# Optimization experiments

Measured on AMD Instinct MI355X. Metric: run time of the kernel, lower is better.

The kernel has to match this reference:

```python
import jax, jax.numpy as jnp
import numpy as np

ALPHA = 2.0   # ATan surrogate sharpness (spikingjelly default)
V_TH = 1.0    # spike threshold

@jax.custom_vjp
def spike(v):
    # Heaviside spike at threshold V_TH
    return (v >= V_TH).astype(v.dtype)

def _spike_fwd(v):
    return spike(v), v

def _spike_bwd(v, g):
    # ATan surrogate gradient
    sg = (ALPHA / 2.0) / (1.0 + (jnp.pi / 2.0 * ALPHA * (v - V_TH)) ** 2)
    return (g * sg,)

spike.defvjp(_spike_fwd, _spike_bwd)

N, T, D_IN, HID, D_OUT = 512, 1000, 128, 128, 20

def _linear_params(k, fan_in, fan_out):
    # matches torch nn.Linear default init: U(-1/sqrt(fan_in), 1/sqrt(fan_in))
    s = 1.0 / np.sqrt(fan_in)
    kw, kb = jax.random.split(k)
    W = jax.random.uniform(kw, (fan_out, fan_in), minval=-s, maxval=s, dtype=jnp.float32)
    b = jax.random.uniform(kb, (fan_out,), minval=-s, maxval=s, dtype=jnp.float32)
    return W, b

def setup_inputs() -> dict:
    key = jax.random.key(0)
    kx, k1, k2, k3, k4, k5 = jax.random.split(key, 6)
    x = jax.random.normal(kx, (N, T, D_IN), dtype=jnp.float32)
    Wi1, bi1 = _linear_params(k1, D_IN, HID)   # i2h_1
    Wh1, bh1 = _linear_params(k2, HID, HID)    # h2h_1
    Wi2, bi2 = _linear_params(k3, HID, HID)    # i2h_2
    Wh2, bh2 = _linear_params(k4, HID, HID)    # h2h_2
    Wo,  bo  = _linear_params(k5, HID, D_OUT)  # h2o_2
    return {"x": x, "Wi1": Wi1, "bi1": bi1, "Wh1": Wh1, "bh1": bh1,
            "Wi2": Wi2, "bi2": bi2, "Wh2": Wh2, "bh2": bh2, "Wo": Wo, "bo": bo}

def reference(x, Wi1, bi1, Wh1, bh1, Wi2, bi2, Wh2, bh2, Wo, bo):
    n, t = x.shape[0], x.shape[1]
    s1_0 = jnp.zeros((n, Wh1.shape[0]), dtype=x.dtype)
    s2_0 = jnp.zeros((n, Wh2.shape[0]), dtype=x.dtype)
    acc0 = jnp.zeros((n, Wo.shape[0]), dtype=x.dtype)

    def step(carry, xt):
        s1, s2, acc = carry
        h1 = xt @ Wi1.T + bi1 + s1 @ Wh1.T + bh1
        s1 = spike(h1)
        h2 = s1 @ Wi2.T + bi2 + s2 @ Wh2.T + bh2
        s2 = spike(h2)
        acc = acc + s2 @ Wo.T + bo
        return (s1, s2, acc), None

    # scan over time: x -> [T, N, D_IN]
    (_, _, acc), _ = jax.lax.scan(step, (s1_0, s2_0, acc0), jnp.swapaxes(x, 0, 1))
    return acc / t
```

## Files before the change

### kernel.cpp

```cpp
#include <hip/hip_runtime.h>
#include <cstdint>
#include <cstddef>

#define T_STEPS 1000
#define NS      512
#define HID     128
#define DOUT    20
#define XPAD    129
#define PSTR    130
#define SPMM_R  32

extern "C" __global__ void __launch_bounds__(512, 1)
srnn_dense(const float* __restrict__ x, const float* __restrict__ Wi1,
           float* __restrict__ D, int t0, int Tc)
{
    extern __shared__ float sm[];
    float* xs = sm;
    float* Wl = sm + 128 * XPAD;
    const int tid = threadIdx.x;
    const int w = tid >> 6, ln = tid & 63;
    const int rb = blockIdx.x * 128;

    for (int i = tid; i < HID * HID / 4; i += 512)
        ((float4*)Wl)[i] = ((const float4*)Wi1)[i];
    for (int i = tid; i < 128 * 32; i += 512) {
        int r = i >> 5, kq = i & 31;
        int cr = rb + r;
        int s = cr / Tc, trel = cr - s * Tc;
        float4 v = ((const float4*)x)[((size_t)s * T_STEPS + t0 + trel) * 32 + kq];
        float* dst = &xs[r * XPAD + 4 * kq];
        dst[0] = v.x; dst[1] = v.y; dst[2] = v.z; dst[3] = v.w;
    }
    __syncthreads();

    const float* xr0 = xs + ln * XPAD;
    const float* xr1 = xs + (64 + ln) * XPAD;
    for (int og = 0; og < 4; ++og) {
        const int o = 16 * w + 4 * og;
        float a[2][4][4];
        #pragma unroll
        for (int r = 0; r < 2; ++r)
            #pragma unroll
            for (int j = 0; j < 4; ++j)
                #pragma unroll
                for (int i = 0; i < 4; ++i) a[r][j][i] = 0.f;

        #pragma unroll 4
        for (int k = 0; k < HID; k += 4) {
            float4 wv[4];
            #pragma unroll
            for (int j = 0; j < 4; ++j)
                wv[j] = *(const float4*)&Wl[(o + j) * HID + k];
            float xa0[4], xa1[4];
            #pragma unroll
            for (int i = 0; i < 4; ++i) { xa0[i] = xr0[k + i]; xa1[i] = xr1[k + i]; }
            #pragma unroll
            for (int j = 0; j < 4; ++j) {
                a[0][j][0] = fmaf(xa0[0], wv[j].x, a[0][j][0]);
                a[0][j][1] = fmaf(xa0[1], wv[j].y, a[0][j][1]);
                a[0][j][2] = fmaf(xa0[2], wv[j].z, a[0][j][2]);
                a[0][j][3] = fmaf(xa0[3], wv[j].w, a[0][j][3]);
                a[1][j][0] = fmaf(xa1[0], wv[j].x, a[1][j][0]);
                a[1][j][1] = fmaf(xa1[1], wv[j].y, a[1][j][1]);
                a[1][j][2] = fmaf(xa1[2], wv[j].z, a[1][j][2]);
                a[1][j][3] = fmaf(xa1[3], wv[j].w, a[1][j][3]);
            }
        }
        #pragma unroll
        for (int r = 0; r < 2; ++r) {
            float4 dv;
            dv.x = (a[r][0][0] + a[r][0][1]) + (a[r][0][2] + a[r][0][3]);
            dv.y = (a[r][1][0] + a[r][1][1]) + (a[r][1][2] + a[r][1][3]);
            dv.z = (a[r][2][0] + a[r][2][1]) + (a[r][2][2] + a[r][2][3]);
            dv.w = (a[r][3][0] + a[r][3][1]) + (a[r][3][2] + a[r][3][3]);
            *(float4*)&D[(size_t)(rb + 64 * r + ln) * HID + o] = dv;
        }
    }
}

__device__ __forceinline__ void stage_paired(float* __restrict__ WT2,
                                             const float* __restrict__ W,
                                             int tid, int nthreads)
{
    for (int i = tid; i < HID * HID / 4; i += nthreads) {
        int o = i >> 5, jq = i & 31;
        float4 v = ((const float4*)W)[i];
        int c = 2 * (o & 63) + (o >> 6);
        WT2[(4 * jq + 0) * PSTR + c] = v.x;
        WT2[(4 * jq + 1) * PSTR + c] = v.y;
        WT2[(4 * jq + 2) * PSTR + c] = v.z;
        WT2[(4 * jq + 3) * PSTR + c] = v.w;
    }
    for (int i = tid; i < PSTR; i += nthreads) WT2[128 * PSTR + i] = 0.f;
}

__device__ __forceinline__ void sparse4p(const float* __restrict__ WT2,
                                         unsigned long long mm, int base,
                                         int ln2, float& rl, float& rh)
{
    while (mm) {
        int j0 = (int)__builtin_ctzll(mm) + base;            mm &= mm - 1;
        int j1 = mm ? (int)__builtin_ctzll(mm) + base : 128; mm &= mm - 1;
        int j2 = mm ? (int)__builtin_ctzll(mm) + base : 128; mm &= mm - 1;
        int j3 = mm ? (int)__builtin_ctzll(mm) + base : 128; mm &= mm - 1;
        float2 p0 = *(const float2*)&WT2[j0 * PSTR + ln2];
        float2 p1 = *(const float2*)&WT2[j1 * PSTR + ln2];
        float2 p2 = *(const float2*)&WT2[j2 * PSTR + ln2];
        float2 p3 = *(const float2*)&WT2[j3 * PSTR + ln2];
        rl += p0.x; rl += p1.x; rl += p2.x; rl += p3.x;
        rh += p0.y; rh += p1.y; rh += p2.y; rh += p3.y;
    }
}

extern "C" __global__ void __launch_bounds__(128, 1)
srnn_recur1(const float* __restrict__ Dn, const float* __restrict__ Wh,
            const float* __restrict__ bi, const float* __restrict__ bh,
            ulonglong2* __restrict__ masks, ulonglong2* __restrict__ state,
            int t0, int Tc, int first)
{
    extern __shared__ float WT2[];
    const int tid = threadIdx.x, w = tid >> 6, ln = tid & 63, ln2 = 2 * ln;
    const int s = 2 * blockIdx.x + w;

    stage_paired(WT2, Wh, tid, 128);

    const float bil = bi[ln], bih = bi[64 + ln];
    const float bhl = bh[ln], bhh = bh[64 + ln];
    unsigned long long m0 = 0ULL, m1 = 0ULL;
    if (!first) { ulonglong2 st = state[s]; m0 = st.x; m1 = st.y; }

    const float* Drow = Dn + (size_t)s * Tc * HID;
    float dl[8], dh[8];
    #pragma unroll
    for (int p = 0; p < 8; ++p) {
        int ti = p < Tc ? p : Tc - 1;
        dl[p] = Drow[ti * HID + ln];
        dh[p] = Drow[ti * HID + 64 + ln];
    }
    __syncthreads();

    for (int tt = 0; tt < Tc; tt += 8) {
        #pragma unroll
        for (int u = 0; u < 8; ++u) {
            int t = tt + u;
            if (t >= Tc) break;
            float dense_l = dl[u], dense_h = dh[u];
            int tp = (t + 8 < Tc) ? t + 8 : Tc - 1;
            dl[u] = Drow[tp * HID + ln];
            dh[u] = Drow[tp * HID + 64 + ln];

            float rl = 0.f, rh = 0.f;
            sparse4p(WT2, m0, 0,  ln2, rl, rh);
            sparse4p(WT2, m1, 64, ln2, rl, rh);

            float hl = ((dense_l + bil) + rl) + bhl;
            float hh = ((dense_h + bih) + rh) + bhh;
            m0 = __ballot(hl >= 1.0f);
            m1 = __ballot(hh >= 1.0f);
            if (ln == 0) {
                ulonglong2 mv; mv.x = m0; mv.y = m1;
                masks[(size_t)s * T_STEPS + (t0 + t)] = mv;
            }
        }
    }
    if (ln == 0) { ulonglong2 st; st.x = m0; st.y = m1; state[s] = st; }
}

extern "C" __global__ void __launch_bounds__(256, 1)
srnn_spmm(const ulonglong2* __restrict__ masks1, const float* __restrict__ Wi2,
          float* __restrict__ D2, int t0, int Tc)
{
    extern __shared__ float WI2[];
    const int tid = threadIdx.x, w = tid >> 6, ln = tid & 63, ln2 = 2 * ln;
    stage_paired(WI2, Wi2, tid, 256);
    __syncthreads();

    const int s = blockIdx.y;
    const int tbase = (blockIdx.x * 4 + w) * SPMM_R;
    if (tbase >= Tc) return;
    const ulonglong2* mrow = masks1 + (size_t)s * T_STEPS + t0;

    ulonglong2 m = mrow[tbase];
    for (int r = 0; r < SPMM_R; ++r) {
        int trel = tbase + r;
        if (trel >= Tc) break;
        ulonglong2 cm = m;
        if (r + 1 < SPMM_R && trel + 1 < Tc) m = mrow[trel + 1];

        float Al = 0.f, Ah = 0.f;
        sparse4p(WI2, cm.x, 0,  ln2, Al, Ah);
        sparse4p(WI2, cm.y, 64, ln2, Al, Ah);

        size_t ro = ((size_t)s * Tc + trel) * HID;
        D2[ro + ln] = Al;
        D2[ro + 64 + ln] = Ah;
    }
}

extern "C" __global__ void __launch_bounds__(128, 1)
srnn_recur2(const float* __restrict__ D2, const float* __restrict__ Wh2,
            const float* __restrict__ bi2, const float* __restrict__ bh2,
            const float* __restrict__ Wo,  const float* __restrict__ bo,
            ulonglong2* __restrict__ state, float* __restrict__ accst,
            float* __restrict__ out, int t0, int Tc, int first, int last)
{
    extern __shared__ float sm2[];
    float* WT2 = sm2;
    float* WOt = sm2 + 129 * PSTR;
    const int tid = threadIdx.x, w = tid >> 6, ln = tid & 63, ln2 = 2 * ln;
    const int s = 2 * blockIdx.x + w;

    stage_paired(WT2, Wh2, tid, 128);
    for (int i = tid; i < DOUT * HID / 4; i += 128) {
        int o = i >> 5, jq = i & 31;
        float4 v = ((const float4*)Wo)[i];
        WOt[(4 * jq + 0) * DOUT + o] = v.x; WOt[(4 * jq + 1) * DOUT + o] = v.y;
        WOt[(4 * jq + 2) * DOUT + o] = v.z; WOt[(4 * jq + 3) * DOUT + o] = v.w;
    }
    for (int i = tid; i < DOUT; i += 128) WOt[128 * DOUT + i] = 0.f;

    const float bil = bi2[ln], bih = bi2[64 + ln];
    const float bhl = bh2[ln], bhh = bh2[64 + ln];
    const bool  oth = (ln < DOUT);
    const float bov = oth ? bo[ln] : 0.f;
    unsigned long long p0 = 0ULL, p1 = 0ULL;
    float acc = 0.f;
    if (!first) {
        ulonglong2 st = state[s]; p0 = st.x; p1 = st.y;
        if (oth) acc = accst[s * DOUT + ln];
    }

    const float* Drow = D2 + (size_t)s * Tc * HID;
    float dl[8], dh[8];
    #pragma unroll
    for (int p = 0; p < 8; ++p) {
        int ti = p < Tc ? p : Tc - 1;
        dl[p] = Drow[ti * HID + ln];
        dh[p] = Drow[ti * HID + 64 + ln];
    }
    __syncthreads();

    for (int tt = 0; tt < Tc; tt += 8) {
        #pragma unroll
        for (int u = 0; u < 8; ++u) {
            int t = tt + u;
            if (t >= Tc) break;
            float Al = dl[u], Ah = dh[u];
            int tp = (t + 8 < Tc) ? t + 8 : Tc - 1;
            dl[u] = Drow[tp * HID + ln];
            dh[u] = Drow[tp * HID + 64 + ln];

            float Bl = 0.f, Bh = 0.f;
            sparse4p(WT2, p0, 0,  ln2, Bl, Bh);
            sparse4p(WT2, p1, 64, ln2, Bl, Bh);

            float hl = ((Al + bil) + Bl) + bhl;
            float hh = ((Ah + bih) + Bh) + bhh;
            p0 = __ballot(hl >= 1.0f);
            p1 = __ballot(hh >= 1.0f);

            if (oth) {
                float d = 0.f;
                unsigned long long mm = p0;
                while (mm) {
                    int j0 = (int)__builtin_ctzll(mm);       mm &= mm - 1;
                    int j1 = mm ? (int)__builtin_ctzll(mm) : 128; mm &= mm - 1;
                    int j2 = mm ? (int)__builtin_ctzll(mm) : 128; mm &= mm - 1;
                    int j3 = mm ? (int)__builtin_ctzll(mm) : 128; mm &= mm - 1;
                    float w0 = WOt[j0 * DOUT + ln], w1 = WOt[j1 * DOUT + ln];
                    float w2 = WOt[j2 * DOUT + ln], w3 = WOt[j3 * DOUT + ln];
                    d += w0; d += w1; d += w2; d += w3;
                }
                mm = p1;
                while (mm) {
                    int j0 = 64 + (int)__builtin_ctzll(mm);       mm &= mm - 1;
                    int j1 = mm ? 64 + (int)__builtin_ctzll(mm) : 128; mm &= mm - 1;
                    int j2 = mm ? 64 + (int)__builtin_ctzll(mm) : 128; mm &= mm - 1;
                    int j3 = mm ? 64 + (int)__builtin_ctzll(mm) : 128; mm &= mm - 1;
                    float w0 = WOt[j0 * DOUT + ln], w1 = WOt[j1 * DOUT + ln];
                    float w2 = WOt[j2 * DOUT + ln], w3 = WOt[j3 * DOUT + ln];
                    d += w0; d += w1; d += w2; d += w3;
                }
                acc += d;
                acc += bov;
            }
        }
    }
    if (ln == 0) { ulonglong2 st; st.x = p0; st.y = p1; state[s] = st; }
    if (oth) {
        if (last) out[s * DOUT + ln] = acc / (float)T_STEPS;
        else      accst[s * DOUT + ln] = acc;
    }
}

extern "C" void kernel_launch(void* const* d_in, const int* in_sizes, int n_in,
                              void* d_out, int out_size, void* d_ws, size_t ws_size,
                              hipStream_t stream) {
    const float* x   = (const float*)d_in[0];
    const float* Wi1 = (const float*)d_in[1];
    const float* bi1 = (const float*)d_in[2];
    const float* Wh1 = (const float*)d_in[3];
    const float* bh1 = (const float*)d_in[4];
    const float* Wi2 = (const float*)d_in[5];
    const float* bi2 = (const float*)d_in[6];
    const float* Wh2 = (const float*)d_in[7];
    const float* bh2 = (const float*)d_in[8];
    const float* Wo  = (const float*)d_in[9];
    const float* bo  = (const float*)d_in[10];
    float* out = (float*)d_out;

    const size_t mb = (size_t)NS * T_STEPS * sizeof(ulonglong2);
    ulonglong2* masks1 = (ulonglong2*)d_ws;
    ulonglong2* state  = (ulonglong2*)((char*)d_ws + mb);
    const size_t state_bytes = (size_t)2 * NS * sizeof(ulonglong2);
    float* accst = (float*)((char*)d_ws + mb + state_bytes);
    const size_t acc_bytes = (size_t)NS * DOUT * sizeof(float);
    float* Dbuf = (float*)((char*)d_ws + mb + state_bytes + acc_bytes);

    const size_t base = mb + state_bytes + acc_bytes;
    size_t avail = ws_size > base ? ws_size - base : 0;
    const size_t bytes_per_t = (size_t)NS * HID * sizeof(float);
    long tcmax = (long)(avail / bytes_per_t);
    static const int divs[] = {1000, 500, 250, 200, 125, 100, 50, 40, 25, 20, 10, 8, 5, 4, 2, 1};
    int Tc = 1;
    for (int i = 0; i < 16; ++i) if (divs[i] <= tcmax) { Tc = divs[i]; break; }

    const int lds0 = (128 * XPAD + HID * HID) * (int)sizeof(float);
    const int ldsP = (129 * PSTR) * (int)sizeof(float);
    const int lds2 = (129 * PSTR + 129 * DOUT) * (int)sizeof(float);
    hipFuncSetAttribute((const void*)srnn_dense,
                        hipFuncAttributeMaxDynamicSharedMemorySize, lds0);
    hipFuncSetAttribute((const void*)srnn_recur1,
                        hipFuncAttributeMaxDynamicSharedMemorySize, ldsP);
    hipFuncSetAttribute((const void*)srnn_spmm,
                        hipFuncAttributeMaxDynamicSharedMemorySize, ldsP);
    hipFuncSetAttribute((const void*)srnn_recur2,
                        hipFuncAttributeMaxDynamicSharedMemorySize, lds2);

    for (int t0 = 0; t0 < T_STEPS; t0 += Tc) {
        srnn_dense<<<4 * Tc, 512, lds0, stream>>>(x, Wi1, Dbuf, t0, Tc);
        srnn_recur1<<<NS / 2, 128, ldsP, stream>>>(Dbuf, Wh1, bi1, bh1,
                                                   masks1, state, t0, Tc, t0 == 0);
    }
    for (int t0 = 0; t0 < T_STEPS; t0 += Tc) {
        dim3 g2((Tc + 4 * SPMM_R - 1) / (4 * SPMM_R), NS);
        srnn_spmm<<<g2, 256, ldsP, stream>>>(masks1, Wi2, Dbuf, t0, Tc);
        srnn_recur2<<<NS / 2, 128, lds2, stream>>>(Dbuf, Wh2, bi2, bh2, Wo, bo,
                                                   state + NS, accst, out,
                                                   t0, Tc, t0 == 0,
                                                   t0 + Tc >= T_STEPS);
    }
}
```

Measured before the change: 1.800 ms.

## Software-pipeline sparse recurrent gathers by issuing next-step weight loads right after ballot

The two recurrent kernels now walk the spike bits of both mask halves through one merged iterator. Right after each ballot they gather the first eight weight rows for the next step, so those LDS loads overlap the mask store, the output accumulation and the next dense-input prefetch. The output projection in layer two reuses the same indices and hoists its first eight loads. The dense prefetch depth drops from 8 to 4 in a rolling register window, and Tc is limited to multiples of 4 to match the unroll. The register pressure is higher, and inactive lanes now run the output loop with a clamped column index.

```diff
diff --git a/kernel.cpp b/kernel.cpp
--- a/kernel.cpp
+++ b/kernel.cpp
@@ -94,6 +94,13 @@
     for (int i = tid; i < PSTR; i += nthreads) WT2[128 * PSTR + i] = 0.f;
 }
 
+__device__ __forceinline__ int popnext(unsigned long long& a, unsigned long long& b)
+{
+    if (a) { int j = (int)__builtin_ctzll(a); a &= a - 1; return j; }
+    if (b) { int j = 64 + (int)__builtin_ctzll(b); b &= b - 1; return j; }
+    return 128;
+}
+
 __device__ __forceinline__ void sparse4p(const float* __restrict__ WT2,
                                          unsigned long long mm, int base,
                                          int ln2, float& rl, float& rh)
@@ -128,40 +135,73 @@
     const float bhl = bh[ln], bhh = bh[64 + ln];
     unsigned long long m0 = 0ULL, m1 = 0ULL;
     if (!first) { ulonglong2 st = state[s]; m0 = st.x; m1 = st.y; }
+    __syncthreads();
 
     const float* Drow = Dn + (size_t)s * Tc * HID;
-    float dl[8], dh[8];
-    #pragma unroll
-    for (int p = 0; p < 8; ++p) {
-        int ti = p < Tc ? p : Tc - 1;
-        dl[p] = Drow[ti * HID + ln];
-        dh[p] = Drow[ti * HID + 64 + ln];
-    }
-    __syncthreads();
-
-    for (int tt = 0; tt < Tc; tt += 8) {
-        #pragma unroll
-        for (int u = 0; u < 8; ++u) {
-            int t = tt + u;
-            if (t >= Tc) break;
-            float dense_l = dl[u], dense_h = dh[u];
-            int tp = (t + 8 < Tc) ? t + 8 : Tc - 1;
-            dl[u] = Drow[tp * HID + ln];
-            dh[u] = Drow[tp * HID + 64 + ln];
-
-            float rl = 0.f, rh = 0.f;
-            sparse4p(WT2, m0, 0,  ln2, rl, rh);
-            sparse4p(WT2, m1, 64, ln2, rl, rh);
-
-            float hl = ((dense_l + bil) + rl) + bhl;
-            float hh = ((dense_h + bih) + rh) + bhh;
-            m0 = __ballot(hl >= 1.0f);
-            m1 = __ballot(hh >= 1.0f);
-            if (ln == 0) {
-                ulonglong2 mv; mv.x = m0; mv.y = m1;
-                masks[(size_t)s * T_STEPS + (t0 + t)] = mv;
-            }
-        }
+    const int i1 = 1 < Tc ? 1 : Tc - 1;
+    const int i2 = 2 < Tc ? 2 : Tc - 1;
+    const int i3 = 3 < Tc ? 3 : Tc - 1;
+    float cl0 = Drow[ln],            ch0 = Drow[64 + ln];
+    float cl1 = Drow[i1 * HID + ln], ch1 = Drow[i1 * HID + 64 + ln];
+    float cl2 = Drow[i2 * HID + ln], ch2 = Drow[i2 * HID + 64 + ln];
+    float cl3 = Drow[i3 * HID + ln], ch3 = Drow[i3 * HID + 64 + ln];
+
+    unsigned long long a = m0, b = m1;
+    int j0 = popnext(a, b), j1 = popnext(a, b), j2 = popnext(a, b), j3 = popnext(a, b);
+    int j4 = popnext(a, b), j5 = popnext(a, b), j6 = popnext(a, b), j7 = popnext(a, b);
+    float2 v0 = *(const float2*)&WT2[j0 * PSTR + ln2];
+    float2 v1 = *(const float2*)&WT2[j1 * PSTR + ln2];
+    float2 v2 = *(const float2*)&WT2[j2 * PSTR + ln2];
+    float2 v3 = *(const float2*)&WT2[j3 * PSTR + ln2];
+    float2 v4 = *(const float2*)&WT2[j4 * PSTR + ln2];
+    float2 v5 = *(const float2*)&WT2[j5 * PSTR + ln2];
+    float2 v6 = *(const float2*)&WT2[j6 * PSTR + ln2];
+    float2 v7 = *(const float2*)&WT2[j7 * PSTR + ln2];
+    unsigned long long ra = a, rb = b;
+
+    #pragma unroll 4
+    for (int t = 0; t < Tc; ++t) {
+        float rl = 0.f, rh = 0.f;
+        rl += v0.x; rl += v1.x; rl += v2.x; rl += v3.x;
+        rl += v4.x; rl += v5.x; rl += v6.x; rl += v7.x;
+        rh += v0.y; rh += v1.y; rh += v2.y; rh += v3.y;
+        rh += v4.y; rh += v5.y; rh += v6.y; rh += v7.y;
+        while (ra | rb) {
+            int k0 = popnext(ra, rb), k1 = popnext(ra, rb);
+            int k2 = popnext(ra, rb), k3 = popnext(ra, rb);
+            float2 q0 = *(const float2*)&WT2[k0 * PSTR + ln2];
+            float2 q1 = *(const float2*)&WT2[k1 * PSTR + ln2];
+            float2 q2 = *(const float2*)&WT2[k2 * PSTR + ln2];
+            float2 q3 = *(const float2*)&WT2[k3 * PSTR + ln2];
+            rl += q0.x; rl += q1.x; rl += q2.x; rl += q3.x;
+            rh += q0.y; rh += q1.y; rh += q2.y; rh += q3.y;
+        }
+
+        float hl = ((cl0 + bil) + rl) + bhl;
+        float hh = ((ch0 + bih) + rh) + bhh;
+        m0 = __ballot(hl >= 1.0f);
+        m1 = __ballot(hh >= 1.0f);
+        if (ln == 0) {
+            ulonglong2 mv; mv.x = m0; mv.y = m1;
+            masks[(size_t)s * T_STEPS + (t0 + t)] = mv;
+        }
+
+        a = m0; b = m1;
+        j0 = popnext(a, b); j1 = popnext(a, b); j2 = popnext(a, b); j3 = popnext(a, b);
+        j4 = popnext(a, b); j5 = popnext(a, b); j6 = popnext(a, b); j7 = popnext(a, b);
+        v0 = *(const float2*)&WT2[j0 * PSTR + ln2];
+        v1 = *(const float2*)&WT2[j1 * PSTR + ln2];
+        v2 = *(const float2*)&WT2[j2 * PSTR + ln2];
+        v3 = *(const float2*)&WT2[j3 * PSTR + ln2];
+        v4 = *(const float2*)&WT2[j4 * PSTR + ln2];
+        v5 = *(const float2*)&WT2[j5 * PSTR + ln2];
+        v6 = *(const float2*)&WT2[j6 * PSTR + ln2];
+        v7 = *(const float2*)&WT2[j7 * PSTR + ln2];
+        ra = a; rb = b;
+
+        cl0 = cl1; ch0 = ch1; cl1 = cl2; ch1 = ch2; cl2 = cl3; ch2 = ch3;
+        int tn = (t + 4 < Tc) ? t + 4 : Tc - 1;
+        cl3 = Drow[tn * HID + ln]; ch3 = Drow[tn * HID + 64 + ln];
     }
     if (ln == 0) { ulonglong2 st; st.x = m0; st.y = m1; state[s] = st; }
 }
@@ -222,6 +262,7 @@
     const float bil = bi2[ln], bih = bi2[64 + ln];
     const float bhl = bh2[ln], bhh = bh2[64 + ln];
     const bool  oth = (ln < DOUT);
+    const int   c   = oth ? ln : 0;
     const float bov = oth ? bo[ln] : 0.f;
     unsigned long long p0 = 0ULL, p1 = 0ULL;
     float acc = 0.f;
@@ -229,62 +270,85 @@
         ulonglong2 st = state[s]; p0 = st.x; p1 = st.y;
         if (oth) acc = accst[s * DOUT + ln];
     }
+    __syncthreads();
 
     const float* Drow = D2 + (size_t)s * Tc * HID;
-    float dl[8], dh[8];
-    #pragma unroll
-    for (int p = 0; p < 8; ++p) {
-        int ti = p < Tc ? p : Tc - 1;
-        dl[p] = Drow[ti * HID + ln];
-        dh[p] = Drow[ti * HID + 64 + ln];
-    }
-    __syncthreads();
-
-    for (int tt = 0; tt < Tc; tt += 8) {
-        #pragma unroll
-        for (int u = 0; u < 8; ++u) {
-            int t = tt + u;
-            if (t >= Tc) break;
-            float Al = dl[u], Ah = dh[u];
-            int tp = (t + 8 < Tc) ? t + 8 : Tc - 1;
-            dl[u] = Drow[tp * HID + ln];
-            dh[u] = Drow[tp * HID + 64 + ln];
-
-            float Bl = 0.f, Bh = 0.f;
-            sparse4p(WT2, p0, 0,  ln2, Bl, Bh);
-            sparse4p(WT2, p1, 64, ln2, Bl, Bh);
-
-            float hl = ((Al + bil) + Bl) + bhl;
-            float hh = ((Ah + bih) + Bh) + bhh;
-            p0 = __ballot(hl >= 1.0f);
-            p1 = __ballot(hh >= 1.0f);
-
-            if (oth) {
-                float d = 0.f;
-                unsigned long long mm = p0;
-                while (mm) {
-                    int j0 = (int)__builtin_ctzll(mm);       mm &= mm - 1;
-                    int j1 = mm ? (int)__builtin_ctzll(mm) : 128; mm &= mm - 1;
-                    int j2 = mm ? (int)__builtin_ctzll(mm) : 128; mm &= mm - 1;
-                    int j3 = mm ? (int)__builtin_ctzll(mm) : 128; mm &= mm - 1;
-                    float w0 = WOt[j0 * DOUT + ln], w1 = WOt[j1 * DOUT + ln];
-                    float w2 = WOt[j2 * DOUT + ln], w3 = WOt[j3 * DOUT + ln];
-                    d += w0; d += w1; d += w2; d += w3;
-                }
-                mm = p1;
-                while (mm) {
-                    int j0 = 64 + (int)__builtin_ctzll(mm);       mm &= mm - 1;
-                    int j1 = mm ? 64 + (int)__builtin_ctzll(mm) : 128; mm &= mm - 1;
-                    int j2 = mm ? 64 + (int)__builtin_ctzll(mm) : 128; mm &= mm - 1;
-                    int j3 = mm ? 64 + (int)__builtin_ctzll(mm) : 128; mm &= mm - 1;
-                    float w0 = WOt[j0 * DOUT + ln], w1 = WOt[j1 * DOUT + ln];
-                    float w2 = WOt[j2 * DOUT + ln], w3 = WOt[j3 * DOUT + ln];
-                    d += w0; d += w1; d += w2; d += w3;
-                }
-                acc += d;
-                acc += bov;
-            }
-        }
+    const int i1 = 1 < Tc ? 1 : Tc - 1;
+    const int i2 = 2 < Tc ? 2 : Tc - 1;
+    const int i3 = 3 < Tc ? 3 : Tc - 1;
+    float cl0 = Drow[ln],            ch0 = Drow[64 + ln];
+    float cl1 = Drow[i1 * HID + ln], ch1 = Drow[i1 * HID + 64 + ln];
+    float cl2 = Drow[i2 * HID + ln], ch2 = Drow[i2 * HID + 64 + ln];
+    float cl3 = Drow[i3 * HID + ln], ch3 = Drow[i3 * HID + 64 + ln];
+
+    unsigned long long a = p0, b = p1;
+    int j0 = popnext(a, b), j1 = popnext(a, b), j2 = popnext(a, b), j3 = popnext(a, b);
+    int j4 = popnext(a, b), j5 = popnext(a, b), j6 = popnext(a, b), j7 = popnext(a, b);
+    float2 v0 = *(const float2*)&WT2[j0 * PSTR + ln2];
+    float2 v1 = *(const float2*)&WT2[j1 * PSTR + ln2];
+    float2 v2 = *(const float2*)&WT2[j2 * PSTR + ln2];
+    float2 v3 = *(const float2*)&WT2[j3 * PSTR + ln2];
+    float2 v4 = *(const float2*)&WT2[j4 * PSTR + ln2];
+    float2 v5 = *(const float2*)&WT2[j5 * PSTR + ln2];
+    float2 v6 = *(const float2*)&WT2[j6 * PSTR + ln2];
+    float2 v7 = *(const float2*)&WT2[j7 * PSTR + ln2];
+    unsigned long long ra = a, rb = b;
+
+    #pragma unroll 4
+    for (int t = 0; t < Tc; ++t) {
+        float Bl = 0.f, Bh = 0.f;
+        Bl += v0.x; Bl += v1.x; Bl += v2.x; Bl += v3.x;
+        Bl += v4.x; Bl += v5.x; Bl += v6.x; Bl += v7.x;
+        Bh += v0.y; Bh += v1.y; Bh += v2.y; Bh += v3.y;
+        Bh += v4.y; Bh += v5.y; Bh += v6.y; Bh += v7.y;
+        while (ra | rb) {
+            int k0 = popnext(ra, rb), k1 = popnext(ra, rb);
+            int k2 = popnext(ra, rb), k3 = popnext(ra, rb);
+            float2 q0 = *(const float2*)&WT2[k0 * PSTR + ln2];
+            float2 q1 = *(const float2*)&WT2[k1 * PSTR + ln2];
+            float2 q2 = *(const float2*)&WT2[k2 * PSTR + ln2];
+            float2 q3 = *(const float2*)&WT2[k3 * PSTR + ln2];
+            Bl += q0.x; Bl += q1.x; Bl += q2.x; Bl += q3.x;
+            Bh += q0.y; Bh += q1.y; Bh += q2.y; Bh += q3.y;
+        }
+
+        float hl = ((cl0 + bil) + Bl) + bhl;
+        float hh = ((ch0 + bih) + Bh) + bhh;
+        p0 = __ballot(hl >= 1.0f);
+        p1 = __ballot(hh >= 1.0f);
+
+        a = p0; b = p1;
+        j0 = popnext(a, b); j1 = popnext(a, b); j2 = popnext(a, b); j3 = popnext(a, b);
+        j4 = popnext(a, b); j5 = popnext(a, b); j6 = popnext(a, b); j7 = popnext(a, b);
+        v0 = *(const float2*)&WT2[j0 * PSTR + ln2];
+        v1 = *(const float2*)&WT2[j1 * PSTR + ln2];
+        v2 = *(const float2*)&WT2[j2 * PSTR + ln2];
+        v3 = *(const float2*)&WT2[j3 * PSTR + ln2];
+        v4 = *(const float2*)&WT2[j4 * PSTR + ln2];
+        v5 = *(const float2*)&WT2[j5 * PSTR + ln2];
+        v6 = *(const float2*)&WT2[j6 * PSTR + ln2];
+        v7 = *(const float2*)&WT2[j7 * PSTR + ln2];
+        float u0 = WOt[j0 * DOUT + c], u1 = WOt[j1 * DOUT + c];
+        float u2 = WOt[j2 * DOUT + c], u3 = WOt[j3 * DOUT + c];
+        float u4 = WOt[j4 * DOUT + c], u5 = WOt[j5 * DOUT + c];
+        float u6 = WOt[j6 * DOUT + c], u7 = WOt[j7 * DOUT + c];
+        unsigned long long oa = a, ob = b;
+        ra = a; rb = b;
+
+        float d = 0.f;
+        d += u0; d += u1; d += u2; d += u3; d += u4; d += u5; d += u6; d += u7;
+        while (oa | ob) {
+            int k0 = popnext(oa, ob), k1 = popnext(oa, ob);
+            int k2 = popnext(oa, ob), k3 = popnext(oa, ob);
+            float w0 = WOt[k0 * DOUT + c], w1 = WOt[k1 * DOUT + c];
+            float w2 = WOt[k2 * DOUT + c], w3 = WOt[k3 * DOUT + c];
+            d += w0; d += w1; d += w2; d += w3;
+        }
+        if (oth) { acc += d; acc += bov; }
+
+        cl0 = cl1; ch0 = ch1; cl1 = cl2; ch1 = ch2; cl2 = cl3; ch2 = ch3;
+        int tn = (t + 4 < Tc) ? t + 4 : Tc - 1;
+        cl3 = Drow[tn * HID + ln]; ch3 = Drow[tn * HID + 64 + ln];
     }
     if (ln == 0) { ulonglong2 st; st.x = p0; st.y = p1; state[s] = st; }
     if (oth) {
@@ -321,9 +385,9 @@
     size_t avail = ws_size > base ? ws_size - base : 0;
     const size_t bytes_per_t = (size_t)NS * HID * sizeof(float);
     long tcmax = (long)(avail / bytes_per_t);
-    static const int divs[] = {1000, 500, 250, 200, 125, 100, 50, 40, 25, 20, 10, 8, 5, 4, 2, 1};
-    int Tc = 1;
-    for (int i = 0; i < 16; ++i) if (divs[i] <= tcmax) { Tc = divs[i]; break; }
+    static const int divs[] = {1000, 500, 200, 100, 40, 20, 8, 4};
+    int Tc = 4;
+    for (int i = 0; i < 8; ++i) if (divs[i] <= tcmax) { Tc = divs[i]; break; }
 
     const int lds0 = (128 * XPAD + HID * HID) * (int)sizeof(float);
     const int ldsP = (129 * PSTR) * (int)sizeof(float);
```

New measurement: 2.693 ms. 49.6% more time.

## Interleave four samples per wavefront in recurrent spike kernels

Applied to the files above, without the earlier changes.

Each wavefront in both recurrent kernels now processes four samples at once, interleaving their sparse weight-row gathers so that LDS loads from independent chains can overlap. Blocks grow to 256 threads covering 16 samples, so far fewer workgroups are launched. The dense-input prefetch depth is reduced to two steps, and the chunk-size table is limited to multiples of four. This trades GPU-wide parallelism (many fewer blocks than CUs) for per-wave latency hiding, and each step now waits for the busiest of four samples.

```diff
diff --git a/kernel.cpp b/kernel.cpp
--- a/kernel.cpp
+++ b/kernel.cpp
@@ -9,6 +9,7 @@
 #define XPAD    129
 #define PSTR    130
 #define SPMM_R  32
+#define SPW     4
 
 extern "C" __global__ void __launch_bounds__(512, 1)
 srnn_dense(const float* __restrict__ x, const float* __restrict__ Wi1,
@@ -94,25 +95,57 @@
     for (int i = tid; i < PSTR; i += nthreads) WT2[128 * PSTR + i] = 0.f;
 }
 
+__device__ __forceinline__ void pop4(unsigned long long& mm, int base, int j[4])
+{
+    j[0] = mm ? (int)__builtin_ctzll(mm) + base : 128; mm &= mm - 1;
+    j[1] = mm ? (int)__builtin_ctzll(mm) + base : 128; mm &= mm - 1;
+    j[2] = mm ? (int)__builtin_ctzll(mm) + base : 128; mm &= mm - 1;
+    j[3] = mm ? (int)__builtin_ctzll(mm) + base : 128; mm &= mm - 1;
+}
+
 __device__ __forceinline__ void sparse4p(const float* __restrict__ WT2,
                                          unsigned long long mm, int base,
                                          int ln2, float& rl, float& rh)
 {
     while (mm) {
-        int j0 = (int)__builtin_ctzll(mm) + base;            mm &= mm - 1;
-        int j1 = mm ? (int)__builtin_ctzll(mm) + base : 128; mm &= mm - 1;
-        int j2 = mm ? (int)__builtin_ctzll(mm) + base : 128; mm &= mm - 1;
-        int j3 = mm ? (int)__builtin_ctzll(mm) + base : 128; mm &= mm - 1;
-        float2 p0 = *(const float2*)&WT2[j0 * PSTR + ln2];
-        float2 p1 = *(const float2*)&WT2[j1 * PSTR + ln2];
-        float2 p2 = *(const float2*)&WT2[j2 * PSTR + ln2];
-        float2 p3 = *(const float2*)&WT2[j3 * PSTR + ln2];
+        int j[4]; pop4(mm, base, j);
+        float2 p0 = *(const float2*)&WT2[j[0] * PSTR + ln2];
+        float2 p1 = *(const float2*)&WT2[j[1] * PSTR + ln2];
+        float2 p2 = *(const float2*)&WT2[j[2] * PSTR + ln2];
+        float2 p3 = *(const float2*)&WT2[j[3] * PSTR + ln2];
         rl += p0.x; rl += p1.x; rl += p2.x; rl += p3.x;
         rh += p0.y; rh += p1.y; rh += p2.y; rh += p3.y;
     }
 }
 
-extern "C" __global__ void __launch_bounds__(128, 1)
+__device__ __forceinline__ void sparse_multi(const float* __restrict__ WT2,
+                                             unsigned long long a[SPW], int base,
+                                             int ln2, float rl[SPW], float rh[SPW])
+{
+    while (a[0] | a[1] | a[2] | a[3]) {
+        int j0[4], j1[4], j2[4], j3[4];
+        pop4(a[0], base, j0); pop4(a[1], base, j1);
+        pop4(a[2], base, j2); pop4(a[3], base, j3);
+        float2 p0[4], p1[4], p2[4], p3[4];
+        #pragma unroll
+        for (int k = 0; k < 4; ++k) {
+            p0[k] = *(const float2*)&WT2[j0[k] * PSTR + ln2];
+            p1[k] = *(const float2*)&WT2[j1[k] * PSTR + ln2];
+            p2[k] = *(const float2*)&WT2[j2[k] * PSTR + ln2];
+            p3[k] = *(const float2*)&WT2[j3[k] * PSTR + ln2];
+        }
+        rl[0] += p0[0].x; rl[0] += p0[1].x; rl[0] += p0[2].x; rl[0] += p0[3].x;
+        rh[0] += p0[0].y; rh[0] += p0[1].y; rh[0] += p0[2].y; rh[0] += p0[3].y;
+        rl[1] += p1[0].x; rl[1] += p1[1].x; rl[1] += p1[2].x; rl[1] += p1[3].x;
+        rh[1] += p1[0].y; rh[1] += p1[1].y; rh[1] += p1[2].y; rh[1] += p1[3].y;
+        rl[2] += p2[0].x; rl[2] += p2[1].x; rl[2] += p2[2].x; rl[2] += p2[3].x;
+        rh[2] += p2[0].y; rh[2] += p2[1].y; rh[2] += p2[2].y; rh[2] += p2[3].y;
+        rl[3] += p3[0].x; rl[3] += p3[1].x; rl[3] += p3[2].x; rl[3] += p3[3].x;
+        rh[3] += p3[0].y; rh[3] += p3[1].y; rh[3] += p3[2].y; rh[3] += p3[3].y;
+    }
+}
+
+extern "C" __global__ void __launch_bounds__(256, 1)
 srnn_recur1(const float* __restrict__ Dn, const float* __restrict__ Wh,
             const float* __restrict__ bi, const float* __restrict__ bh,
             ulonglong2* __restrict__ masks, ulonglong2* __restrict__ state,
@@ -120,50 +153,82 @@
 {
     extern __shared__ float WT2[];
     const int tid = threadIdx.x, w = tid >> 6, ln = tid & 63, ln2 = 2 * ln;
-    const int s = 2 * blockIdx.x + w;
-
-    stage_paired(WT2, Wh, tid, 128);
-
+    const int sbase = blockIdx.x * (4 * SPW) + w * SPW;
+
+    stage_paired(WT2, Wh, tid, 256);
     const float bil = bi[ln], bih = bi[64 + ln];
     const float bhl = bh[ln], bhh = bh[64 + ln];
-    unsigned long long m0 = 0ULL, m1 = 0ULL;
-    if (!first) { ulonglong2 st = state[s]; m0 = st.x; m1 = st.y; }
-
-    const float* Drow = Dn + (size_t)s * Tc * HID;
-    float dl[8], dh[8];
-    #pragma unroll
-    for (int p = 0; p < 8; ++p) {
-        int ti = p < Tc ? p : Tc - 1;
-        dl[p] = Drow[ti * HID + ln];
-        dh[p] = Drow[ti * HID + 64 + ln];
+
+    unsigned long long M0[SPW], M1[SPW];
+    #pragma unroll
+    for (int q = 0; q < SPW; ++q) { M0[q] = 0ULL; M1[q] = 0ULL; }
+    if (!first) {
+        #pragma unroll
+        for (int q = 0; q < SPW; ++q) {
+            ulonglong2 st = state[sbase + q]; M0[q] = st.x; M1[q] = st.y;
+        }
     }
     __syncthreads();
 
-    for (int tt = 0; tt < Tc; tt += 8) {
-        #pragma unroll
-        for (int u = 0; u < 8; ++u) {
-            int t = tt + u;
-            if (t >= Tc) break;
-            float dense_l = dl[u], dense_h = dh[u];
-            int tp = (t + 8 < Tc) ? t + 8 : Tc - 1;
-            dl[u] = Drow[tp * HID + ln];
-            dh[u] = Drow[tp * HID + 64 + ln];
-
-            float rl = 0.f, rh = 0.f;
-            sparse4p(WT2, m0, 0,  ln2, rl, rh);
-            sparse4p(WT2, m1, 64, ln2, rl, rh);
-
-            float hl = ((dense_l + bil) + rl) + bhl;
-            float hh = ((dense_h + bih) + rh) + bhh;
-            m0 = __ballot(hl >= 1.0f);
-            m1 = __ballot(hh >= 1.0f);
-            if (ln == 0) {
-                ulonglong2 mv; mv.x = m0; mv.y = m1;
-                masks[(size_t)s * T_STEPS + (t0 + t)] = mv;
-            }
-        }
-    }
-    if (ln == 0) { ulonglong2 st; st.x = m0; st.y = m1; state[s] = st; }
+    const float* Dr[SPW];
+    #pragma unroll
+    for (int q = 0; q < SPW; ++q) Dr[q] = Dn + (size_t)(sbase + q) * Tc * HID;
+
+    float c0l[SPW], c0h[SPW], c1l[SPW], c1h[SPW];
+    const int t1i = (1 < Tc) ? 1 : Tc - 1;
+    #pragma unroll
+    for (int q = 0; q < SPW; ++q) {
+        c0l[q] = Dr[q][ln];                c0h[q] = Dr[q][64 + ln];
+        c1l[q] = Dr[q][t1i * HID + ln];    c1h[q] = Dr[q][t1i * HID + 64 + ln];
+    }
+
+    for (int t = 0; t < Tc; ++t) {
+        const int tn = (t + 2 < Tc) ? t + 2 : Tc - 1;
+        float c2l[SPW], c2h[SPW];
+        #pragma unroll
+        for (int q = 0; q < SPW; ++q) {
+            c2l[q] = Dr[q][tn * HID + ln];
+            c2h[q] = Dr[q][tn * HID + 64 + ln];
+        }
+
+        float rl[SPW], rh[SPW];
+        #pragma unroll
+        for (int q = 0; q < SPW; ++q) { rl[q] = 0.f; rh[q] = 0.f; }
+        unsigned long long a[SPW];
+        #pragma unroll
+        for (int q = 0; q < SPW; ++q) a[q] = M0[q];
+        sparse_multi(WT2, a, 0, ln2, rl, rh);
+        #pragma unroll
+        for (int q = 0; q < SPW; ++q) a[q] = M1[q];
+        sparse_multi(WT2, a, 64, ln2, rl, rh);
+
+        #pragma unroll
+        for (int q = 0; q < SPW; ++q) {
+            float hl = ((c0l[q] + bil) + rl[q]) + bhl;
+            float hh = ((c0h[q] + bih) + rh[q]) + bhh;
+            M0[q] = __ballot(hl >= 1.0f);
+            M1[q] = __ballot(hh >= 1.0f);
+        }
+        unsigned long long lo = M0[0], hi = M1[0];
+        if (ln == 1) { lo = M0[1]; hi = M1[1]; }
+        if (ln == 2) { lo = M0[2]; hi = M1[2]; }
+        if (ln == 3) { lo = M0[3]; hi = M1[3]; }
+        if (ln < SPW) {
+            ulonglong2 mv; mv.x = lo; mv.y = hi;
+            masks[(size_t)(sbase + ln) * T_STEPS + (t0 + t)] = mv;
+        }
+        #pragma unroll
+        for (int q = 0; q < SPW; ++q) {
+            c0l[q] = c1l[q]; c0h[q] = c1h[q];
+            c1l[q] = c2l[q]; c1h[q] = c2h[q];
+        }
+    }
+    if (ln == 0) {
+        #pragma unroll
+        for (int q = 0; q < SPW; ++q) {
+            ulonglong2 st; st.x = M0[q]; st.y = M1[q]; state[sbase + q] = st;
+        }
+    }
 }
 
 extern "C" __global__ void __launch_bounds__(256, 1)
@@ -197,7 +262,7 @@
     }
 }
 
-extern "C" __global__ void __launch_bounds__(128, 1)
+extern "C" __global__ void __launch_bounds__(256, 1)
 srnn_recur2(const float* __restrict__ D2, const float* __restrict__ Wh2,
             const float* __restrict__ bi2, const float* __restrict__ bh2,
             const float* __restrict__ Wo,  const float* __restrict__ bo,
@@ -208,88 +273,127 @@
     float* WT2 = sm2;
     float* WOt = sm2 + 129 * PSTR;
     const int tid = threadIdx.x, w = tid >> 6, ln = tid & 63, ln2 = 2 * ln;
-    const int s = 2 * blockIdx.x + w;
-
-    stage_paired(WT2, Wh2, tid, 128);
-    for (int i = tid; i < DOUT * HID / 4; i += 128) {
+    const int sbase = blockIdx.x * (4 * SPW) + w * SPW;
+
+    stage_paired(WT2, Wh2, tid, 256);
+    for (int i = tid; i < DOUT * HID / 4; i += 256) {
         int o = i >> 5, jq = i & 31;
         float4 v = ((const float4*)Wo)[i];
         WOt[(4 * jq + 0) * DOUT + o] = v.x; WOt[(4 * jq + 1) * DOUT + o] = v.y;
         WOt[(4 * jq + 2) * DOUT + o] = v.z; WOt[(4 * jq + 3) * DOUT + o] = v.w;
     }
-    for (int i = tid; i < DOUT; i += 128) WOt[128 * DOUT + i] = 0.f;
+    for (int i = tid; i < DOUT; i += 256) WOt[128 * DOUT + i] = 0.f;
 
     const float bil = bi2[ln], bih = bi2[64 + ln];
     const float bhl = bh2[ln], bhh = bh2[64 + ln];
     const bool  oth = (ln < DOUT);
+    const int   c   = oth ? ln : 0;
     const float bov = oth ? bo[ln] : 0.f;
-    unsigned long long p0 = 0ULL, p1 = 0ULL;
-    float acc = 0.f;
+
+    unsigned long long M0[SPW], M1[SPW];
+    float acc[SPW];
+    #pragma unroll
+    for (int q = 0; q < SPW; ++q) { M0[q] = 0ULL; M1[q] = 0ULL; acc[q] = 0.f; }
     if (!first) {
-        ulonglong2 st = state[s]; p0 = st.x; p1 = st.y;
-        if (oth) acc = accst[s * DOUT + ln];
-    }
-
-    const float* Drow = D2 + (size_t)s * Tc * HID;
-    float dl[8], dh[8];
-    #pragma unroll
-    for (int p = 0; p < 8; ++p) {
-        int ti = p < Tc ? p : Tc - 1;
-        dl[p] = Drow[ti * HID + ln];
-        dh[p] = Drow[ti * HID + 64 + ln];
+        #pragma unroll
+        for (int q = 0; q < SPW; ++q) {
+            ulonglong2 st = state[sbase + q]; M0[q] = st.x; M1[q] = st.y;
+            if (oth) acc[q] = accst[(sbase + q) * DOUT + ln];
+        }
     }
     __syncthreads();
 
-    for (int tt = 0; tt < Tc; tt += 8) {
-        #pragma unroll
-        for (int u = 0; u < 8; ++u) {
-            int t = tt + u;
-            if (t >= Tc) break;
-            float Al = dl[u], Ah = dh[u];
-            int tp = (t + 8 < Tc) ? t + 8 : Tc - 1;
-            dl[u] = Drow[tp * HID + ln];
-            dh[u] = Drow[tp * HID + 64 + ln];
-
-            float Bl = 0.f, Bh = 0.f;
-            sparse4p(WT2, p0, 0,  ln2, Bl, Bh);
-            sparse4p(WT2, p1, 64, ln2, Bl, Bh);
-
-            float hl = ((Al + bil) + Bl) + bhl;
-            float hh = ((Ah + bih) + Bh) + bhh;
-            p0 = __ballot(hl >= 1.0f);
-            p1 = __ballot(hh >= 1.0f);
-
-            if (oth) {
-                float d = 0.f;
-                unsigned long long mm = p0;
-                while (mm) {
-                    int j0 = (int)__builtin_ctzll(mm);       mm &= mm - 1;
-                    int j1 = mm ? (int)__builtin_ctzll(mm) : 128; mm &= mm - 1;
-                    int j2 = mm ? (int)__builtin_ctzll(mm) : 128; mm &= mm - 1;
-                    int j3 = mm ? (int)__builtin_ctzll(mm) : 128; mm &= mm - 1;
-                    float w0 = WOt[j0 * DOUT + ln], w1 = WOt[j1 * DOUT + ln];
-                    float w2 = WOt[j2 * DOUT + ln], w3 = WOt[j3 * DOUT + ln];
-                    d += w0; d += w1; d += w2; d += w3;
+    const float* Dr[SPW];
+    #pragma unroll
+    for (int q = 0; q < SPW; ++q) Dr[q] = D2 + (size_t)(sbase + q) * Tc * HID;
+
+    float c0l[SPW], c0h[SPW], c1l[SPW], c1h[SPW];
+    const int t1i = (1 < Tc) ? 1 : Tc - 1;
+    #pragma unroll
+    for (int q = 0; q < SPW; ++q) {
+        c0l[q] = Dr[q][ln];                c0h[q] = Dr[q][64 + ln];
+        c1l[q] = Dr[q][t1i * HID + ln];    c1h[q] = Dr[q][t1i * HID + 64 + ln];
+    }
+
+    for (int t = 0; t < Tc; ++t) {
+        const int tn = (t + 2 < Tc) ? t + 2 : Tc - 1;
+        float c2l[SPW], c2h[SPW];
+        #pragma unroll
+        for (int q = 0; q < SPW; ++q) {
+            c2l[q] = Dr[q][tn * HID + ln];
+            c2h[q] = Dr[q][tn * HID + 64 + ln];
+        }
+
+        float Bl[SPW], Bh[SPW];
+        #pragma unroll
+        for (int q = 0; q < SPW; ++q) { Bl[q] = 0.f; Bh[q] = 0.f; }
+        unsigned long long a[SPW];
+        #pragma unroll
+        for (int q = 0; q < SPW; ++q) a[q] = M0[q];
+        sparse_multi(WT2, a, 0, ln2, Bl, Bh);
+        #pragma unroll
+        for (int q = 0; q < SPW; ++q) a[q] = M1[q];
+        sparse_multi(WT2, a, 64, ln2, Bl, Bh);
+
+        #pragma unroll
+        for (int q = 0; q < SPW; ++q) {
+            float hl = ((c0l[q] + bil) + Bl[q]) + bhl;
+            float hh = ((c0h[q] + bih) + Bh[q]) + bhh;
+            M0[q] = __ballot(hl >= 1.0f);
+            M1[q] = __ballot(hh >= 1.0f);
+        }
+
+        float d[SPW];
+        #pragma unroll
+        for (int q = 0; q < SPW; ++q) d[q] = 0.f;
+        #pragma unroll
+        for (int half = 0; half < 2; ++half) {
+            unsigned long long b0 = half ? M1[0] : M0[0];
+            unsigned long long b1 = half ? M1[1] : M0[1];
+            unsigned long long b2 = half ? M1[2] : M0[2];
+            unsigned long long b3 = half ? M1[3] : M0[3];
+            const int base = half ? 64 : 0;
+            while (b0 | b1 | b2 | b3) {
+                int j0[4], j1[4], j2[4], j3[4];
+                pop4(b0, base, j0); pop4(b1, base, j1);
+                pop4(b2, base, j2); pop4(b3, base, j3);
+                float w0[4], w1[4], w2[4], w3[4];
+                #pragma unroll
+                for (int k = 0; k < 4; ++k) {
+                    w0[k] = WOt[j0[k] * DOUT + c];
+                    w1[k] = WOt[j1[k] * DOUT + c];
+                    w2[k] = WOt[j2[k] * DOUT + c];
+                    w3[k] = WOt[j3[k] * DOUT + c];
                 }
-                mm = p1;
-                while (mm) {
-                    int j0 = 64 + (int)__builtin_ctzll(mm);       mm &= mm - 1;
-                    int j1 = mm ? 64 + (int)__builtin_ctzll(mm) : 128; mm &= mm - 1;
-                    int j2 = mm ? 64 + (int)__builtin_ctzll(mm) : 128; mm &= mm - 1;
-                    int j3 = mm ? 64 + (int)__builtin_ctzll(mm) : 128; mm &= mm - 1;
-                    float w0 = WOt[j0 * DOUT + ln], w1 = WOt[j1 * DOUT + ln];
-                    float w2 = WOt[j2 * DOUT + ln], w3 = WOt[j3 * DOUT + ln];
-                    d += w0; d += w1; d += w2; d += w3;
-                }
-                acc += d;
-                acc += bov;
+                d[0] += w0[0]; d[0] += w0[1]; d[0] += w0[2]; d[0] += w0[3];
+                d[1] += w1[0]; d[1] += w1[1]; d[1] += w1[2]; d[1] += w1[3];
+                d[2] += w2[0]; d[2] += w2[1]; d[2] += w2[2]; d[2] += w2[3];
+                d[3] += w3[0]; d[3] += w3[1]; d[3] += w3[2]; d[3] += w3[3];
             }
         }
-    }
-    if (ln == 0) { ulonglong2 st; st.x = p0; st.y = p1; state[s] = st; }
+        #pragma unroll
+        for (int q = 0; q < SPW; ++q) {
+            if (oth) { acc[q] += d[q]; acc[q] += bov; }
+        }
+
+        #pragma unroll
+        for (int q = 0; q < SPW; ++q) {
+            c0l[q] = c1l[q]; c0h[q] = c1h[q];
+            c1l[q] = c2l[q]; c1h[q] = c2h[q];
+        }
+    }
+    if (ln == 0) {
+        #pragma unroll
+        for (int q = 0; q < SPW; ++q) {
+            ulonglong2 st; st.x = M0[q]; st.y = M1[q]; state[sbase + q] = st;
+        }
+    }
     if (oth) {
-        if (last) out[s * DOUT + ln] = acc / (float)T_STEPS;
-        else      accst[s * DOUT + ln] = acc;
+        #pragma unroll
+        for (int q = 0; q < SPW; ++q) {
+            if (last) out[(sbase + q) * DOUT + ln] = acc[q] / (float)T_STEPS;
+            else      accst[(sbase + q) * DOUT + ln] = acc[q];
+        }
     }
 }
 
@@ -321,9 +425,9 @@
     size_t avail = ws_size > base ? ws_size - base : 0;
     const size_t bytes_per_t = (size_t)NS * HID * sizeof(float);
     long tcmax = (long)(avail / bytes_per_t);
-    static const int divs[] = {1000, 500, 250, 200, 125, 100, 50, 40, 25, 20, 10, 8, 5, 4, 2, 1};
-    int Tc = 1;
-    for (int i = 0; i < 16; ++i) if (divs[i] <= tcmax) { Tc = divs[i]; break; }
+    static const int divs[] = {1000, 500, 200, 100, 40, 20, 8, 4};
+    int Tc = 4;
+    for (int i = 0; i < 8; ++i) if (divs[i] <= tcmax) { Tc = divs[i]; break; }
 
     const int lds0 = (128 * XPAD + HID * HID) * (int)sizeof(float);
     const int ldsP = (129 * PSTR) * (int)sizeof(float);
@@ -337,17 +441,19 @@
     hipFuncSetAttribute((const void*)srnn_recur2,
                         hipFuncAttributeMaxDynamicSharedMemorySize, lds2);
 
+    const int rblocks = NS / (4 * SPW);
+
     for (int t0 = 0; t0 < T_STEPS; t0 += Tc) {
         srnn_dense<<<4 * Tc, 512, lds0, stream>>>(x, Wi1, Dbuf, t0, Tc);
-        srnn_recur1<<<NS / 2, 128, ldsP, stream>>>(Dbuf, Wh1, bi1, bh1,
-                                                   masks1, state, t0, Tc, t0 == 0);
+        srnn_recur1<<<rblocks, 256, ldsP, stream>>>(Dbuf, Wh1, bi1, bh1,
+                                                    masks1, state, t0, Tc, t0 == 0);
     }
     for (int t0 = 0; t0 < T_STEPS; t0 += Tc) {
         dim3 g2((Tc + 4 * SPMM_R - 1) / (4 * SPMM_R), NS);
         srnn_spmm<<<g2, 256, ldsP, stream>>>(masks1, Wi2, Dbuf, t0, Tc);
-        srnn_recur2<<<NS / 2, 128, lds2, stream>>>(Dbuf, Wh2, bi2, bh2, Wo, bo,
-                                                   state + NS, accst, out,
-                                                   t0, Tc, t0 == 0,
-                                                   t0 + Tc >= T_STEPS);
-    }
-}
+        srnn_recur2<<<rblocks, 256, lds2, stream>>>(Dbuf, Wh2, bi2, bh2, Wo, bo,
+                                                    state + NS, accst, out,
+                                                    t0, Tc, t0 == 0,
+                                                    t0 + Tc >= T_STEPS);
+    }
+}
```

Result: slower. 3.432 ms (+90.6%).
